# Optimization experiments

Hardware: AMD Instinct MI355X
Metric: run time of the kernel (lower is better)

## Reference

```python
import jax, jax.numpy as jnp
import numpy as np

THRESH = 0.5
DECAY = 0.2
D_IN = 784
H1 = 2048
H2 = 10
K = 10
U = D_IN + H1
L = 128
B = 1024


def setup_inputs() -> dict:
    key = jax.random.key(0)
    ks = jax.random.split(key, 6)
    inp = jax.random.uniform(ks[0], (B, D_IN), dtype=jnp.float32)
    W1 = jax.random.normal(ks[1], (H1, D_IN), dtype=jnp.float32) * 0.05
    b1 = jnp.zeros((H1,), dtype=jnp.float32)
    W2 = jax.random.normal(ks[2], (H2, H1), dtype=jnp.float32) * 0.05
    b2 = jnp.zeros((H2,), dtype=jnp.float32)
    # core_mem_all[k][u][0] -> sparse-ish per-unit vector, [1] -> count
    core_mem_vec = (jax.random.uniform(ks[3], (K, U, L)) > 0.7).astype(jnp.float32)
    core_mem_cnt = jax.random.randint(ks[4], (K, U), 0, 5).astype(jnp.int32)
    return {"input": inp, "W1": W1, "b1": b1, "W2": W2, "b2": b2,
            "core_mem_vec": core_mem_vec, "core_mem_cnt": core_mem_cnt,
            "time_window": 20}


def act_fun(mem):
    # spike = Heaviside(mem - thresh)
    return (mem > THRESH).astype(mem.dtype)


def reference(input, W1, b1, W2, b2, core_mem_vec, core_mem_cnt, time_window):
    batch, d_in = input.shape
    h1 = W1.shape[0]
    h2 = W2.shape[0]
    Lv = core_mem_vec.shape[-1]

    # Precompute, per (core k, unit u): contribution to count_add_1 / count_add_2
    # when unit u spikes. count_add_1 += (last nonzero index of temp) - 1 when cnt>0;
    # count_add_2 += cnt when cnt>0. Sum over cores up front (loop order irrelevant).
    nz = core_mem_vec != 0                                     # [K,U,L]
    has = nz.any(-1)
    last_idx = Lv - 1 - jnp.argmax(nz[..., ::-1].astype(jnp.int32), axis=-1)  # [K,U]
    active = (core_mem_cnt > 0) & has
    val1 = jnp.where(active, last_idx - 1, 0).sum(0).astype(jnp.float32)      # [U]
    val2 = jnp.where(core_mem_cnt > 0, core_mem_cnt, 0).sum(0).astype(jnp.float32)
    v1x, v1h = val1[:d_in], val1[d_in:]
    v2x, v2h = val2[:d_in], val2[d_in:]

    key = jax.random.key(42)

    def step(carry, t):
        h1m, h1s, h2m, h2s, h2sum, a1, a2, cs = carry
        # Bernoulli rate encoding of the input image
        x = (input > jax.random.uniform(jax.random.fold_in(key, t), input.shape)).astype(jnp.float32)
        # mem_update: mem = mem*decay*(1-spike) + W x + b ; spike = mem > thresh
        h1m = h1m * DECAY * (1.0 - h1s) + x @ W1.T + b1
        h1s = act_fun(h1m)
        h2m = h2m * DECAY * (1.0 - h2s) + h1s @ W2.T + b2
        h2s = act_fun(h2m)
        h2sum = h2sum + h2s
        # vectorized core-memory gather/count: sum per-unit precomputed values
        # over all spiking units, across the batch
        xs = x.sum(0)      # [784] spike counts per input unit this step
        hs = h1s.sum(0)    # [h1]
        a1 = a1 + xs @ v1x + hs @ v1h
        a2 = a2 + xs @ v2x + hs @ v2h
        cs = cs + xs.sum() + hs.sum()
        return (h1m, h1s, h2m, h2s, h2sum, a1, a2, cs), None

    z1 = jnp.zeros((batch, h1), dtype=jnp.float32)
    z2 = jnp.zeros((batch, h2), dtype=jnp.float32)
    carry = (z1, z1, z2, z2, z2, jnp.float32(0), jnp.float32(0), jnp.float32(0))
    carry, _ = jax.lax.scan(step, carry, jnp.arange(time_window))
    _, _, _, _, h2sum, a1, a2, cs = carry
    outputs = h2sum / time_window
    return outputs, a1, a2, cs
```

## Files before the change

kernel.cpp:

```cpp
#include <hip/hip_runtime.h>
#include <cstdint>
#include <cstddef>

static constexpr int D_IN = 784;
static constexpr int H1   = 2048;
static constexpr int H2   = 10;
static constexpr int KK   = 10;
static constexpr int UU   = 2832;
static constexpr int LL   = 128;
static constexpr int BB   = 1024;
static constexpr int TT   = 20;
static constexpr int HALF = BB * D_IN / 2;
static constexpr int KS   = 13;
static constexpr int NLIMB = 3;
static constexpr int NT16 = 128;
static constexpr int MT16 = 64;
static constexpr int PANEL16 = KS * NLIMB * 64;
static constexpr int NPART = 512;
static constexpr int NGENB = 2080;

static constexpr int BLK_VALS  = UU / 4;
static constexpr int BLK_W2T   = H1 / 256;
static constexpr int BLK_LIMBS = (NT16 * KS) / 4;
static constexpr int PREP_BLOCKS = BLK_VALS + BLK_W2T + BLK_LIMBS + NGENB;

typedef int v4i  __attribute__((ext_vector_type(4)));

#define MFMA16 __builtin_amdgcn_mfma_i32_16x16x64_i8

__device__ __forceinline__ uint32_t rotl32(uint32_t x, int d) {
  return (x << d) | (x >> (32 - d));
}
__device__ __forceinline__ void threefry2x32(uint32_t k0, uint32_t k1,
                                             uint32_t& x0, uint32_t& x1) {
  uint32_t ks2 = k0 ^ k1 ^ 0x1BD11BDAu;
  x0 += k0; x1 += k1;
#define TF_R(r) { x0 += x1; x1 = rotl32(x1, (r)); x1 ^= x0; }
  TF_R(13) TF_R(15) TF_R(26) TF_R(6)
  x0 += k1;  x1 += ks2 + 1u;
  TF_R(17) TF_R(29) TF_R(16) TF_R(24)
  x0 += ks2; x1 += k0 + 2u;
  TF_R(13) TF_R(15) TF_R(26) TF_R(6)
  x0 += k0;  x1 += k1 + 3u;
  TF_R(17) TF_R(29) TF_R(16) TF_R(24)
  x0 += k1;  x1 += ks2 + 4u;
  TF_R(13) TF_R(15) TF_R(26) TF_R(6)
  x0 += ks2; x1 += k0 + 5u;
#undef TF_R
}
__device__ __forceinline__ float bits_to_unif(uint32_t b) {
  uint32_t fb = (b >> 9) | 0x3F800000u;
  return __uint_as_float(fb) - 1.0f;
}

__device__ __forceinline__ double wave_red(double v) {
  #pragma unroll
  for (int off = 32; off > 0; off >>= 1) v += __shfl_down(v, off, 64);
  return v;
}
__device__ __forceinline__ void block_store3(double s0, double s1, double s2,
                                             double* slot) {
  __shared__ double lds[3][8];
  int lane = threadIdx.x & 63, w = threadIdx.x >> 6;
  int nw = (int)(blockDim.x >> 6);
  s0 = wave_red(s0); s1 = wave_red(s1); s2 = wave_red(s2);
  if (lane == 0) { lds[0][w] = s0; lds[1][w] = s1; lds[2][w] = s2; }
  __syncthreads();
  if (threadIdx.x == 0) {
    double t0 = 0, t1 = 0, t2 = 0;
    for (int i = 0; i < nw; i++) { t0 += lds[0][i]; t1 += lds[1][i]; t2 += lds[2][i]; }
    slot[0] = t0; slot[1] = t1; slot[2] = t2;
  }
}

__global__ __launch_bounds__(256)
void prep(const float* __restrict__ cmv, const int* __restrict__ cmc,
          float* __restrict__ v1, float* __restrict__ v2,
          const float* __restrict__ W2, float* __restrict__ W2T,
          const float* __restrict__ W1, v4i* __restrict__ W1L,
          const float* __restrict__ input, v4i* __restrict__ XA,
          int* __restrict__ xcp) {
  int bx = blockIdx.x;
  if (bx < BLK_VALS) {
    int u = bx * 4 + (threadIdx.x >> 6);
    int lane = threadIdx.x & 63;
    float acc1 = 0.0f, acc2 = 0.0f;
    for (int k = 0; k < KK; k++) {
      const float* p = cmv + ((size_t)k * UU + u) * LL;
      float a = p[lane];
      float b = p[lane + 64];
      unsigned long long mlo = __ballot(a != 0.0f);
      unsigned long long mhi = __ballot(b != 0.0f);
      int c = cmc[k * UU + u];
      if (c > 0) {
        int last = mhi ? (127 - __builtin_clzll(mhi))
                       : (mlo ? (63 - __builtin_clzll(mlo)) : -1);
        if (last >= 0) acc1 += (float)(last - 1);
        acc2 += (float)c;
      }
    }
    if (lane == 0) { v1[u] = acc1; v2[u] = acc2; }
  } else if (bx < BLK_VALS + BLK_W2T) {
    int i = (bx - BLK_VALS) * 256 + threadIdx.x;
    #pragma unroll
    for (int j = 0; j < H2; j++) W2T[i * H2 + j] = W2[j * H1 + i];
  } else if (bx < BLK_VALS + BLK_W2T + BLK_LIMBS) {
    int tid = (bx - BLK_VALS - BLK_W2T) * 256 + threadIdx.x;
    int lane = tid & 63;
    int tw = tid >> 6;
    int nt = tw / KS, s = tw - nt * KS;
    int n = (nt << 4) + (lane & 15);
    int k0 = (s << 6) + ((lane >> 4) << 4);
    bool valid = (k0 < D_IN);
    union { v4i v; signed char b[16]; } d[NLIMB];
    #pragma unroll
    for (int j = 0; j < 16; j++) {
      long long F = 0;
      if (valid) {
        double w = (double)W1[(size_t)n * D_IN + k0 + j];
        F = llround(w * 0x1p24);
        if (F >  8355711LL) F =  8355711LL;
        if (F < -8421504LL) F = -8421504LL;
      }
      #pragma unroll
      for (int l = 0; l < NLIMB; l++) {
        int dig = (int)((F + 128) & 255) - 128;
        d[l].b[j] = (signed char)dig;
        F = (F - dig) >> 8;
      }
    }
    #pragma unroll
    for (int l = 0; l < NLIMB; l++)
      W1L[(size_t)((nt * KS + s) * NLIMB + l) * 64 + lane] = d[l].v;
  } else {
    int gb = bx - (BLK_VALS + BLK_W2T + BLK_LIMBS);
    int s = gb % 13, grp = gb / 13;
    int w = threadIdx.x >> 6, lane = threadIdx.x & 63;
    int task = grp * 4 + w;
    int t = task >> 5, mt = task & 31;
    int m = (mt << 4) + (lane & 15);
    int g = lane >> 4;
    int k0 = (s << 6) + (g << 4);
    bool valid = (k0 < D_IN);
    __shared__ int xc[64];
    if (threadIdx.x < 64) xc[threadIdx.x] = 0;
    __syncthreads();
    uint32_t f0 = 0u, f1 = (uint32_t)t;
    threefry2x32(0u, 42u, f0, f1);
    const float4* P0 = (const float4*)(input + (valid ? (size_t)m * D_IN + k0 : 0));
    const float4* P1 = (const float4*)(input + (valid ? (size_t)(m + 512) * D_IN + k0 : 0));
    float i0v[16], i1v[16];
    #pragma unroll
    for (int q = 0; q < 4; q++) {
      float4 a4 = P0[q], b4 = P1[q];
      i0v[q * 4 + 0] = a4.x; i0v[q * 4 + 1] = a4.y;
      i0v[q * 4 + 2] = a4.z; i0v[q * 4 + 3] = a4.w;
      i1v[q * 4 + 0] = b4.x; i1v[q * 4 + 1] = b4.y;
      i1v[q * 4 + 2] = b4.z; i1v[q * 4 + 3] = b4.w;
    }
    union { v4i v; unsigned char b[16]; } r0, r1;
    #pragma unroll
    for (int j = 0; j < 16; j++) {
      int k = k0 + j;
      uint32_t c0 = (uint32_t)(m * D_IN + k), c1 = c0 + (uint32_t)HALF;
      threefry2x32(f0, f1, c0, c1);
      float u0 = bits_to_unif(c0), u1 = bits_to_unif(c1);
      bool x0 = valid && (i0v[j] > u0);
      bool x1 = valid && (i1v[j] > u1);
      r0.b[j] = x0 ? 1 : 0;
      r1.b[j] = x1 ? 1 : 0;
      unsigned long long bm0 = __ballot(x0);
      unsigned long long bm1 = __ballot(x1);
      if ((lane & 15) == 0) {
        int cnt = __popc((uint32_t)((bm0 >> (g * 16)) & 0xFFFFu))
                + __popc((uint32_t)((bm1 >> (g * 16)) & 0xFFFFu));
        if (cnt) atomicAdd(&xc[(g << 4) + j], cnt);
      }
    }
    XA[(size_t)((t * MT16 + mt) * KS + s) * 64 + lane] = r0.v;
    XA[(size_t)((t * MT16 + mt + 32) * KS + s) * 64 + lane] = r1.v;
    __syncthreads();
    if (threadIdx.x < 64) xcp[(size_t)gb * 64 + threadIdx.x] = xc[threadIdx.x];
  }
}

__global__ __launch_bounds__(512, 4)
void h1_all(const v4i* __restrict__ XA, const v4i* __restrict__ W1L,
            const float* __restrict__ b1, uint16_t* __restrict__ bits16,
            const float* __restrict__ v1, const float* __restrict__ v2,
            const int* __restrict__ xcp, double* __restrict__ gpart) {
  extern __shared__ v4i bl[];
  int lane = threadIdx.x & 63, wv = threadIdx.x >> 6;
  int id = blockIdx.x + (blockIdx.y << 6);
  int xcd = id & 7;
  int ntb = ((id >> 3) << 1) | (xcd >> 2);
  int mg = xcd & 3;
  int mt0 = (mg << 4) + (wv << 1);
  {
    const v4i* wp = W1L + (size_t)ntb * PANEL16;
    for (int i = threadIdx.x; i < PANEL16; i += 512) bl[i] = wp[i];
  }
  __syncthreads();

  int col = lane & 15;
  int gn = (ntb << 4) + col;
  float bias = b1[gn];
  double v1n = (double)v1[D_IN + gn], v2n = (double)v2[D_IN + gn];
  int scnt = 0;
  float m00 = 0, m01 = 0, m02 = 0, m03 = 0;
  float m10 = 0, m11 = 0, m12 = 0, m13 = 0;
  const v4i* bq = bl + lane;
  int rowg = (lane >> 4) << 2;

  #pragma unroll 1
  for (int t = 0; t < TT; t++) {
    const v4i* a0 = XA + (size_t)((t * MT16 + mt0) * KS) * 64 + lane;
    const v4i* a1 = a0 + KS * 64;
    v4i c00 = {}, c01 = {}, c02 = {};
    v4i c10 = {}, c11 = {}, c12 = {};
    __builtin_amdgcn_s_setprio(1);
    #pragma unroll
    for (int s = 0; s < KS; s++) {
      v4i A0 = a0[s * 64], A1 = a1[s * 64];
      v4i B0 = bq[(s * NLIMB + 0) * 64];
      v4i B1 = bq[(s * NLIMB + 1) * 64];
      v4i B2 = bq[(s * NLIMB + 2) * 64];
      c00 = MFMA16(A0, B0, c00, 0, 0, 0);
      c10 = MFMA16(A1, B0, c10, 0, 0, 0);
      c01 = MFMA16(A0, B1, c01, 0, 0, 0);
      c11 = MFMA16(A1, B1, c11, 0, 0, 0);
      c02 = MFMA16(A0, B2, c02, 0, 0, 0);
      c12 = MFMA16(A1, B2, c12, 0, 0, 0);
    }
    __builtin_amdgcn_s_setprio(0);
    #pragma unroll
    for (int tile = 0; tile < 2; tile++) {
      const v4i& q0 = tile ? c10 : c00;
      const v4i& q1 = tile ? c11 : c01;
      const v4i& q2 = tile ? c12 : c02;
      int gmb = ((mt0 + tile) << 4);
      uint16_t* bp = bits16 + ((size_t)t * BB + gmb) * NT16 + ntb;
      #pragma unroll
      for (int r = 0; r < 4; r++) {
        int val = (int)((uint32_t)q0[r] + ((uint32_t)q1[r] << 8)
                        + ((uint32_t)q2[r] << 16));
        float dot = (float)val * 0x1p-24f + bias;
        float mp = tile ? (r == 0 ? m10 : r == 1 ? m11 : r == 2 ? m12 : m13)
                        : (r == 0 ? m00 : r == 1 ? m01 : r == 2 ? m02 : m03);
        float mnew = (mp > 0.5f) ? dot : fmaf(mp, 0.2f, dot);
        bool sp = (mnew > 0.5f);
        if (tile) { if (r == 0) m10 = mnew; else if (r == 1) m11 = mnew;
                    else if (r == 2) m12 = mnew; else m13 = mnew; }
        else      { if (r == 0) m00 = mnew; else if (r == 1) m01 = mnew;
                    else if (r == 2) m02 = mnew; else m03 = mnew; }
        unsigned long long bm = __ballot(sp);
        if ((lane & 15) == 0)
          bp[(size_t)(rowg + r) * NT16] = (uint16_t)(bm >> lane);
        scnt += sp ? 1 : 0;
      }
    }
  }

  double e0 = 0, e1 = 0, e2 = 0;
  {
    int half = threadIdx.x >> 8;
    int gi = threadIdx.x & 255;
    int k = 2 * id + half;
    int xcv = 0;
    if (id < 416 && gi < 160) {
      int s = k >> 6, q = k & 63;
      xcv = xcp[((size_t)(gi * 13 + s) << 6) + q];
    }
    #pragma unroll
    for (int off = 32; off > 0; off >>= 1) xcv += __shfl_down(xcv, off, 64);
    __shared__ int xcs[8];
    if (lane == 0) xcs[wv] = xcv;
    __syncthreads();
    if (threadIdx.x == 0 && id < 416) {
      int xc0 = xcs[0] + xcs[1] + xcs[2] + xcs[3];
      int xc1 = xcs[4] + xcs[5] + xcs[6] + xcs[7];
      int kk0 = 2 * id, kk1 = 2 * id + 1;
      e0 = (double)xc0 * (double)v1[kk0] + (double)xc1 * (double)v1[kk1];
      e1 = (double)xc0 * (double)v2[kk0] + (double)xc1 * (double)v2[kk1];
      e2 = (double)(xc0 + xc1);
    }
  }
  double sc = (double)scnt;
  block_store3(sc * v1n + e0, sc * v2n + e1, sc + e2, gpart + 3 * (size_t)id);
}

__global__ __launch_bounds__(256)
void h2_all(const uint32_t* __restrict__ bits, const float* __restrict__ W2T,
            const float* __restrict__ b2, const double* __restrict__ gpart,
            float* __restrict__ out) {
  int lane = threadIdx.x & 63, wq = threadIdx.x >> 6;
  int b0 = blockIdx.x * 2;
  float w[8][10];
  #pragma unroll
  for (int c = 0; c < 8; c++) {
    int n = (wq << 9) + (c << 6) + lane;
    #pragma unroll
    for (int j = 0; j < 10; j++) w[c][j] = W2T[(size_t)n * H2 + j];
  }
  float m = 0.0f, sp = 0.0f, sm = 0.0f;
  float b2v = (lane < 10) ? b2[lane] : 0.0f;
  __shared__ float part[4][2][10];
  #pragma unroll 1
  for (int t = 0; t < TT; t++) {
    const uint32_t* bt = bits + (size_t)t * (BB * 64);
    #pragma unroll
    for (int r = 0; r < 2; r++) {
      uint32_t myw = bt[(size_t)(b0 + r) * 64 + (wq << 4) + (lane & 15)];
      float p[10];
      #pragma unroll
      for (int j = 0; j < 10; j++) p[j] = 0.0f;
      #pragma unroll
      for (int c = 0; c < 8; c++) {
        uint32_t wd = __shfl(myw, (c << 1) + (lane >> 5), 64);
        float f = (float)((wd >> (lane & 31)) & 1u);
        #pragma unroll
        for (int j = 0; j < 10; j++) p[j] += f * w[c][j];
      }
      #pragma unroll
      for (int j = 0; j < 10; j++) {
        float v = p[j];
        #pragma unroll
        for (int off = 32; off > 0; off >>= 1) v += __shfl_xor(v, off, 64);
        p[j] = v;
      }
      if (lane == 0) {
        #pragma unroll
        for (int j = 0; j < 10; j++) part[wq][r][j] = p[j];
      }
    }
    __syncthreads();
    if (wq < 2 && lane < 10) {
      float red = part[0][wq][lane] + part[1][wq][lane]
                + part[2][wq][lane] + part[3][wq][lane];
      m = m * 0.2f * (1.0f - sp) + red + b2v;
      sp = (m > 0.5f) ? 1.0f : 0.0f;
      sm += sp;
    }
    __syncthreads();
  }
  if (wq < 2 && lane < 10)
    out[(size_t)(b0 + wq) * H2 + lane] = (float)((double)sm / (double)TT);

  if (blockIdx.x == 0) {
    double t0 = 0, t1 = 0, t2 = 0;
    for (int i = threadIdx.x; i < NPART; i += 256) {
      t0 += gpart[3 * (size_t)i];
      t1 += gpart[3 * (size_t)i + 1];
      t2 += gpart[3 * (size_t)i + 2];
    }
    __shared__ double fin[3][4];
    t0 = wave_red(t0); t1 = wave_red(t1); t2 = wave_red(t2);
    if (lane == 0) { fin[0][wq] = t0; fin[1][wq] = t1; fin[2][wq] = t2; }
    __syncthreads();
    if (threadIdx.x == 0) {
      double a = 0, b = 0, cc = 0;
      #pragma unroll
      for (int i = 0; i < 4; i++) { a += fin[0][i]; b += fin[1][i]; cc += fin[2][i]; }
      out[(size_t)BB * H2 + 0] = (float)a;
      out[(size_t)BB * H2 + 1] = (float)b;
      out[(size_t)BB * H2 + 2] = (float)cc;
    }
  }
}

extern "C" void kernel_launch(void* const* d_in, const int* in_sizes, int n_in,
                              void* d_out, int out_size, void* d_ws, size_t ws_size,
                              hipStream_t stream) {
  (void)in_sizes; (void)n_in; (void)out_size; (void)ws_size;
  const float* input = (const float*)d_in[0];
  const float* W1    = (const float*)d_in[1];
  const float* b1    = (const float*)d_in[2];
  const float* W2    = (const float*)d_in[3];
  const float* b2    = (const float*)d_in[4];
  const float* cmv   = (const float*)d_in[5];
  const int*   cmc   = (const int*)d_in[6];

  char* base = (char*)d_ws;
  float*  v1   = (float*)(base + 0);
  float*  v2   = (float*)(base + 11328);
  float*  W2T  = (float*)(base + 22656);
  v4i*    W1L  = (v4i*)(base + 104576);
  v4i*    XA   = (v4i*)(base + 5216384);
  uint16_t* bits16 = (uint16_t*)(base + 22255744);
  int*    xcp  = (int*)(base + 27498624);
  double* gpart = (double*)(base + 28031104);
  const uint32_t* bits32 = (const uint32_t*)(base + 22255744);

  prep<<<PREP_BLOCKS, 256, 0, stream>>>(cmv, cmc, v1, v2, W2, W2T, W1, W1L,
                                        input, XA, xcp);
  h1_all<<<dim3(64, 8), 512, PANEL16 * 16, stream>>>(XA, W1L, b1, bits16, v1, v2,
                                                     xcp, gpart);
  h2_all<<<BB / 2, 256, 0, stream>>>(bits32, W2T, b2, gpart, (float*)d_out);
}
```

Before: 277.7 us.

## Merge pairs of h1 blocks into 1024-thread blocks covering two column panels

The h1 kernel now runs 256 blocks of 1024 threads instead of 512 blocks of 512. Each block loads two adjacent W1 column panels into LDS, and even and odd waves work on different panels while sharing the same input row tiles. The per-block count reduction is reworked for 16 waves and four input-unit slots per block, and NPART is halved to match. The aim is fewer blocks and better reuse of XA loads across the two panels, at the cost of double the LDS per block and possibly lower occupancy or less even load across CUs.

Result: no change. 276.7 us (-0.4%).

```diff
diff --git a/kernel.cpp b/kernel.cpp
--- a/kernel.cpp
+++ b/kernel.cpp
@@ -16,7 +16,7 @@
 static constexpr int NT16 = 128;
 static constexpr int MT16 = 64;
 static constexpr int PANEL16 = KS * NLIMB * 64;
-static constexpr int NPART = 512;
+static constexpr int NPART = 256;
 static constexpr int NGENB = 2080;
 
 static constexpr int BLK_VALS  = UU / 4;
@@ -60,7 +60,7 @@
 }
 __device__ __forceinline__ void block_store3(double s0, double s1, double s2,
                                              double* slot) {
-  __shared__ double lds[3][8];
+  __shared__ double lds[3][16];
   int lane = threadIdx.x & 63, w = threadIdx.x >> 6;
   int nw = (int)(blockDim.x >> 6);
   s0 = wave_red(s0); s1 = wave_red(s1); s2 = wave_red(s2);
@@ -184,7 +184,7 @@
   }
 }
 
-__global__ __launch_bounds__(512, 4)
+__global__ __launch_bounds__(1024, 4)
 void h1_all(const v4i* __restrict__ XA, const v4i* __restrict__ W1L,
             const float* __restrict__ b1, uint16_t* __restrict__ bits16,
             const float* __restrict__ v1, const float* __restrict__ v2,
@@ -193,23 +193,25 @@
   int lane = threadIdx.x & 63, wv = threadIdx.x >> 6;
   int id = blockIdx.x + (blockIdx.y << 6);
   int xcd = id & 7;
-  int ntb = ((id >> 3) << 1) | (xcd >> 2);
+  int nt32 = ((id >> 3) << 1) | (xcd >> 2);
   int mg = xcd & 3;
-  int mt0 = (mg << 4) + (wv << 1);
-  {
-    const v4i* wp = W1L + (size_t)ntb * PANEL16;
-    for (int i = threadIdx.x; i < PANEL16; i += 512) bl[i] = wp[i];
+  int p = wv & 1;
+  int mt0 = (mg << 4) + ((wv >> 1) << 1);
+  for (int i = threadIdx.x; i < 2 * PANEL16; i += 1024) {
+    int pp = (i >= PANEL16) ? 1 : 0;
+    bl[i] = W1L[(size_t)((nt32 << 1) + pp) * PANEL16 + (i - pp * PANEL16)];
   }
   __syncthreads();
 
   int col = lane & 15;
+  int ntb = (nt32 << 1) + p;
   int gn = (ntb << 4) + col;
   float bias = b1[gn];
   double v1n = (double)v1[D_IN + gn], v2n = (double)v2[D_IN + gn];
   int scnt = 0;
   float m00 = 0, m01 = 0, m02 = 0, m03 = 0;
   float m10 = 0, m11 = 0, m12 = 0, m13 = 0;
-  const v4i* bq = bl + lane;
+  const v4i* bq = bl + (size_t)p * PANEL16 + lane;
   int rowg = (lane >> 4) << 2;
 
   #pragma unroll 1
@@ -263,26 +265,28 @@
 
   double e0 = 0, e1 = 0, e2 = 0;
   {
-    int half = threadIdx.x >> 8;
+    int kk = threadIdx.x >> 8;
     int gi = threadIdx.x & 255;
-    int k = 2 * id + half;
+    int k = 4 * id + kk;
     int xcv = 0;
-    if (id < 416 && gi < 160) {
+    if (id < 196 && gi < 160) {
       int s = k >> 6, q = k & 63;
       xcv = xcp[((size_t)(gi * 13 + s) << 6) + q];
     }
     #pragma unroll
     for (int off = 32; off > 0; off >>= 1) xcv += __shfl_down(xcv, off, 64);
-    __shared__ int xcs[8];
+    __shared__ int xcs[16];
     if (lane == 0) xcs[wv] = xcv;
     __syncthreads();
-    if (threadIdx.x == 0 && id < 416) {
-      int xc0 = xcs[0] + xcs[1] + xcs[2] + xcs[3];
-      int xc1 = xcs[4] + xcs[5] + xcs[6] + xcs[7];
-      int kk0 = 2 * id, kk1 = 2 * id + 1;
-      e0 = (double)xc0 * (double)v1[kk0] + (double)xc1 * (double)v1[kk1];
-      e1 = (double)xc0 * (double)v2[kk0] + (double)xc1 * (double)v2[kk1];
-      e2 = (double)(xc0 + xc1);
+    if (threadIdx.x == 0 && id < 196) {
+      #pragma unroll
+      for (int q4 = 0; q4 < 4; q4++) {
+        int xck = xcs[4 * q4] + xcs[4 * q4 + 1] + xcs[4 * q4 + 2] + xcs[4 * q4 + 3];
+        int kk2 = 4 * id + q4;
+        e0 += (double)xck * (double)v1[kk2];
+        e1 += (double)xck * (double)v2[kk2];
+        e2 += (double)xck;
+      }
     }
   }
   double sc = (double)scnt;
@@ -393,7 +397,7 @@
 
   prep<<<PREP_BLOCKS, 256, 0, stream>>>(cmv, cmc, v1, v2, W2, W2T, W1, W1L,
                                         input, XA, xcp);
-  h1_all<<<dim3(64, 8), 512, PANEL16 * 16, stream>>>(XA, W1L, b1, bits16, v1, v2,
-                                                     xcp, gpart);
+  h1_all<<<dim3(64, 4), 1024, 2 * PANEL16 * 16, stream>>>(XA, W1L, b1, bits16,
+                                                          v1, v2, xcp, gpart);
   h2_all<<<BB / 2, 256, 0, stream>>>(bits32, W2T, b2, gpart, (float*)d_out);
 }
```
